# Kernel tuning notes

Measured on AMD Instinct MI355X. Metric: run time of the kernel, lower is better.

Reference implementation:

```python
import jax, jax.numpy as jnp
import numpy as np

B, S, D = 8, 2048, 768        # batch, seq_len, embed_dim
G1, G2, G3 = 16, 16, 16       # grid_shape
L = 768                       # latent_dim
TEMP = 0.5                    # initial temperature (learnable scalar)
GRID_STD = 0.05               # keras 'random_normal' default stddev


def _glorot_uniform(key, fan_in, fan_out):
    lim = jnp.sqrt(6.0 / (fan_in + fan_out))
    return jax.random.uniform(key, (fan_in, fan_out), minval=-lim, maxval=lim, dtype=jnp.float32)


def setup_inputs() -> dict:
    key = jax.random.key(0)
    kx, k1, k2, k3, kg = jax.random.split(key, 5)
    x = jax.random.normal(kx, (B, S, D), dtype=jnp.float32)
    W1 = _glorot_uniform(k1, D, G1)
    W2 = _glorot_uniform(k2, D, G2)
    W3 = _glorot_uniform(k3, D, G3)
    b1 = jnp.zeros((G1,), jnp.float32)
    b2 = jnp.zeros((G2,), jnp.float32)
    b3 = jnp.zeros((G3,), jnp.float32)
    grid = GRID_STD * jax.random.normal(kg, (G1, G2, G3, L), dtype=jnp.float32)
    temperature = jnp.asarray(TEMP, dtype=jnp.float32)
    return {"x": x, "W1": W1, "b1": b1, "W2": W2, "b2": b2,
            "W3": W3, "b3": b3, "grid": grid, "temperature": temperature}


def reference(x, W1, b1, W2, b2, W3, b3, grid, temperature):
    # Flatten (batch, seq) -> tokens, process each token independently (transformer mode)
    b, s, d = x.shape
    xt = x.reshape(b * s, d)                                # (T, D)
    # Per-dimension temperature-controlled softmax addressing distributions
    p1 = jax.nn.softmax((xt @ W1 + b1) / temperature, axis=-1)   # (T, G1)
    p2 = jax.nn.softmax((xt @ W2 + b2) / temperature, axis=-1)   # (T, G2)
    p3 = jax.nn.softmax((xt @ W3 + b3) / temperature, axis=-1)   # (T, G3)
    # Joint probability (outer product) contracted with grid latent vectors:
    # out[t, l] = sum_{i,j,k} p1[t,i] p2[t,j] p3[t,k] grid[i,j,k,l]
    out = jnp.einsum('ti,tj,tk,ijkl->tl', p1, p2, p3, grid, optimize=True)
    return out.reshape(b, s, -1)                            # (B, S, L)
```

## Files before the change

kernel.cpp:

```cpp
#include <hip/hip_runtime.h>
#include <hip/hip_bf16.h>


using f32x2  = __attribute__((ext_vector_type(2))) float;
using f32x4  = __attribute__((ext_vector_type(4))) float;
using f32x16 = __attribute__((ext_vector_type(16))) float;
using half8  = __attribute__((ext_vector_type(8))) _Float16;
using half2v = __attribute__((ext_vector_type(2))) _Float16;
typedef unsigned short ushort_t;
typedef unsigned int uint_t;

typedef const __attribute__((address_space(1))) void* gptr_t;
typedef __attribute__((address_space(3))) void* lptr_t;

#define PSTRIDE 52

static __device__ __forceinline__ ushort_t f2h_bits(float x) {
  union { _Float16 h; ushort_t u; } c;
  c.h = (_Float16)x;
  return c.u;
}

static __device__ __forceinline__ half2v cvt_pkrtz2(float a, float b) {
  auto r = __builtin_amdgcn_cvt_pkrtz(a, b);
  union { decltype(r) i; half2v o; } u;
  u.i = r;
  return u.o;
}

__global__ __launch_bounds__(256) void k_pack(const float* __restrict__ g,
                                              ushort_t* __restrict__ gT,
                                              const float* __restrict__ W1,
                                              const float* __restrict__ W2,
                                              const float* __restrict__ W3,
                                              ushort_t* __restrict__ wfrag) {
  const int tx = threadIdx.x;
  if (blockIdx.y == 12) {
    if (blockIdx.x >= 9) return;
#pragma unroll
    for (int j = 0; j < 16; ++j) {
      const int u = blockIdx.x * 4096 + tx * 16 + j;
      const int e = u & 7;
      const int l = (u >> 3) & 63;
      const int frag = u >> 9;
      const int ks = frag / 3, nf = frag % 3;
      const int d = ks * 32 + 8 * (l >> 4) + e;
      const int col = l & 15;
      const float* Wsel = (nf == 0) ? W1 : (nf == 1) ? W2 : W3;
      wfrag[u] = f2h_bits(Wsel[d * 16 + col]);
    }
    return;
  }
  __shared__ ushort_t tile[64][65];
  const int r0 = blockIdx.x * 64;
  const int c0 = blockIdx.y * 64;
#pragma unroll
  for (int it = 0; it < 4; ++it) {
    const int idx = tx + it * 256;
    const int r = idx >> 4;
    const int c = (idx & 15) << 2;
    const float4 v = *(const float4*)(g + (size_t)(r0 + r) * 768 + (c0 + c));
    tile[c + 0][r] = f2h_bits(v.x);
    tile[c + 1][r] = f2h_bits(v.y);
    tile[c + 2][r] = f2h_bits(v.z);
    tile[c + 3][r] = f2h_bits(v.w);
  }
  __syncthreads();
#pragma unroll
  for (int it = 0; it < 4; ++it) {
    const int idx = tx + it * 256;
    const int r = idx >> 4;
    const int c = (idx & 15) << 2;
    ushort4 o;
    o.x = tile[r][c + 0]; o.y = tile[r][c + 1];
    o.z = tile[r][c + 2]; o.w = tile[r][c + 3];
    *(ushort4*)(gT + (size_t)(c0 + r) * 4096 + (r0 + c)) = o;
  }
}

__global__ __launch_bounds__(256) void k_prep(const float* __restrict__ x,
                                              const ushort_t* __restrict__ wfrag,
                                              const float* __restrict__ b1,
                                              const float* __restrict__ b2,
                                              const float* __restrict__ b3,
                                              const float* __restrict__ temp,
                                              float* __restrict__ p) {
  const int tid = threadIdx.x;
  const int lane = tid & 63;
  const int wv = tid >> 6;
  const int t0w = blockIdx.x * 64 + wv * 16;
  const int m = lane & 15;
  const int q = lane >> 4;

  const float* xrow = x + (size_t)(t0w + m) * 768 + q * 8;

  f32x4 acc[3];
#pragma unroll
  for (int nf = 0; nf < 3; ++nf) acc[nf] = (f32x4){0.f, 0.f, 0.f, 0.f};

  const ushort_t* wf = wfrag + lane * 8;
#pragma unroll
  for (int ks = 0; ks < 24; ++ks) {
    const f32x4 xa = *(const f32x4*)(xrow + ks * 32);
    const f32x4 xb = *(const f32x4*)(xrow + ks * 32 + 4);
    union { half2v h2[4]; half8 h8; } pk;
    pk.h2[0] = cvt_pkrtz2(xa[0], xa[1]);
    pk.h2[1] = cvt_pkrtz2(xa[2], xa[3]);
    pk.h2[2] = cvt_pkrtz2(xb[0], xb[1]);
    pk.h2[3] = cvt_pkrtz2(xb[2], xb[3]);
    const half8 a = pk.h8;
#pragma unroll
    for (int nf = 0; nf < 3; ++nf) {
      const half8 w = *(const half8*)&wf[(size_t)(ks * 3 + nf) * 512];
      acc[nf] = __builtin_amdgcn_mfma_f32_16x16x32_f16(a, w, acc[nf], 0, 0, 0);
    }
  }

  const float invT = 1.0f / temp[0];
  float z[3][4];
  const float bias[3] = {b1[m], b2[m], b3[m]};
#pragma unroll
  for (int nf = 0; nf < 3; ++nf)
#pragma unroll
    for (int r = 0; r < 4; ++r) z[nf][r] = (acc[nf][r] + bias[nf]) * invT;

#pragma unroll
  for (int grp = 0; grp < 3; ++grp) {
    float mx[4], sm[4];
#pragma unroll
    for (int r = 0; r < 4; ++r) mx[r] = z[grp][r];
#pragma unroll
    for (int msk = 1; msk < 16; msk <<= 1)
#pragma unroll
      for (int r = 0; r < 4; ++r) mx[r] = fmaxf(mx[r], __shfl_xor(mx[r], msk));
#pragma unroll
    for (int r = 0; r < 4; ++r) { z[grp][r] = __expf(z[grp][r] - mx[r]); sm[r] = z[grp][r]; }
#pragma unroll
    for (int msk = 1; msk < 16; msk <<= 1)
#pragma unroll
      for (int r = 0; r < 4; ++r) sm[r] += __shfl_xor(sm[r], msk);
#pragma unroll
    for (int r = 0; r < 4; ++r) z[grp][r] /= sm[r];
  }

#pragma unroll
  for (int r = 0; r < 4; ++r) {
    float* prow = p + (size_t)(t0w + 4 * q + r) * PSTRIDE + m;
#pragma unroll
    for (int grp = 0; grp < 3; ++grp) prow[grp * 16] = z[grp][r];
  }
}

__global__ __launch_bounds__(256, 2) void k_gemm(const float* __restrict__ p_g,
                                                 const ushort_t* __restrict__ gT,
                                                 float* __restrict__ out) {
  __shared__ ushort_t Bt[2][192 * 64];
  __shared__ float p1T[16 * 128];

  const int tid = threadIdx.x;
  const int lane = tid & 63;
  const int wv = __builtin_amdgcn_readfirstlane(tid >> 6);
  const int wm = wv >> 1, wn = wv & 1;
  const int g = lane >> 5;
  const int l31 = lane & 31;

  const int f = blockIdx.y * 128 + blockIdx.x;
  const int w = (f & 7) * 64 + (f >> 3);
  const int m0 = (w & 127) * 128;
  const int n0 = (w >> 7) * 192;

  if (tid < 128) {
    const float* pr = p_g + (size_t)(m0 + tid) * PSTRIDE;
#pragma unroll
    for (int qq = 0; qq < 4; ++qq) {
      const f32x4 v = *(const f32x4*)(pr + qq * 4);
#pragma unroll
      for (int e = 0; e < 4; ++e) p1T[(qq * 4 + e) * 128 + tid] = v[e];
    }
  }

  const int rowA0 = m0 + wm * 64 + l31;
  half2v p2h[2][16];
  float p3r[2][8];
#pragma unroll
  for (int mr = 0; mr < 2; ++mr) {
    const float* pr = p_g + (size_t)(rowA0 + mr * 32) * PSTRIDE;
#pragma unroll
    for (int qq = 0; qq < 4; ++qq) {
      const f32x4 v = *(const f32x4*)(pr + 16 + qq * 4);
#pragma unroll
      for (int e = 0; e < 4; ++e)
        p2h[mr][qq * 4 + e] = cvt_pkrtz2(v[e], v[e]);
    }
#pragma unroll
    for (int qq = 0; qq < 2; ++qq) {
      const f32x4 v = *(const f32x4*)(pr + 32 + 8 * g + qq * 4);
      p3r[mr][qq * 4 + 0] = v[0]; p3r[mr][qq * 4 + 1] = v[1];
      p3r[mr][qq * 4 + 2] = v[2]; p3r[mr][qq * 4 + 3] = v[3];
    }
  }

  const int srow = wv * 48 + (lane >> 3);
  const int schunk = (lane & 7) ^ (lane >> 3);
  const ushort_t* sbase = gT + (size_t)(n0 + srow) * 4096 + schunk * 8;
  auto stage = [&](int buf, int kt) {
    const ushort_t* src = sbase + kt * 64;
#pragma unroll
    for (int qq = 0; qq < 6; ++qq) {
      __builtin_amdgcn_global_load_lds((gptr_t)(src + (size_t)qq * 8 * 4096),
                                       (lptr_t)&Bt[buf][(wv * 48 + qq * 8) * 64], 16, 0, 0);
    }
  };

  f32x16 acc[2][3];
#pragma unroll
  for (int mr = 0; mr < 2; ++mr)
#pragma unroll
    for (int nf = 0; nf < 3; ++nf)
#pragma unroll
      for (int e = 0; e < 16; ++e) acc[mr][nf][e] = 0.f;

  stage(0, 0);
  asm volatile("s_waitcnt vmcnt(0) lgkmcnt(0)" ::: "memory");
  __builtin_amdgcn_s_barrier();

  const int rowLoc0 = wm * 64 + l31;
  for (int io = 0; io < 16; ++io) {
    half2v p1p3h[2][4];
#pragma unroll
    for (int mr = 0; mr < 2; ++mr) {
      const float p1v = p1T[io * 128 + rowLoc0 + mr * 32];
#pragma unroll
      for (int qq = 0; qq < 4; ++qq)
        p1p3h[mr][qq] = cvt_pkrtz2(p1v * p3r[mr][2 * qq],
                                   p1v * p3r[mr][2 * qq + 1]);
    }
#pragma unroll
    for (int kq = 0; kq < 4; ++kq) {
      const int kt = io * 4 + kq;
      const ushort_t* bbuf = Bt[kq & 1];

      half8 b[4][3];
#pragma unroll
      for (int s = 0; s < 4; ++s) {
        const int cd = 2 * s + g;
#pragma unroll
        for (int nf = 0; nf < 3; ++nf) {
          const int r = wn * 96 + nf * 32 + l31;
          b[s][nf] = *(const half8*)&bbuf[r * 64 + ((cd ^ (r & 7)) << 3)];
        }
      }
      if (kq < 3 || io < 15) stage((kq + 1) & 1, kt + 1);

#pragma unroll
      for (int s = 0; s < 4; ++s) {
        const int j = kq * 4 + s;
        half8 a[2];
#pragma unroll
        for (int mr = 0; mr < 2; ++mr) {
          union { half2v h2[4]; half8 h8; } pk;
#pragma unroll
          for (int qq = 0; qq < 4; ++qq) pk.h2[qq] = p2h[mr][j] * p1p3h[mr][qq];
          a[mr] = pk.h8;
        }
        __builtin_amdgcn_s_setprio(1);
#pragma unroll
        for (int mr = 0; mr < 2; ++mr)
#pragma unroll
          for (int nf = 0; nf < 3; ++nf)
            acc[mr][nf] = __builtin_amdgcn_mfma_f32_32x32x16_f16(a[mr], b[s][nf], acc[mr][nf], 0, 0, 0);
        __builtin_amdgcn_s_setprio(0);
      }
      asm volatile("s_waitcnt vmcnt(0)" ::: "memory");
      __builtin_amdgcn_s_barrier();
    }
  }

#pragma unroll
  for (int mr = 0; mr < 2; ++mr)
#pragma unroll
    for (int nf = 0; nf < 3; ++nf)
#pragma unroll
      for (int reg = 0; reg < 16; ++reg) {
        const int row = (reg & 3) + 8 * (reg >> 2) + 4 * g;
        const int t = m0 + wm * 64 + mr * 32 + row;
        out[(size_t)t * 768 + n0 + wn * 96 + nf * 32 + l31] = acc[mr][nf][reg];
      }
}

extern "C" void kernel_launch(void* const* d_in, const int* in_sizes, int n_in,
                              void* d_out, int out_size, void* d_ws, size_t ws_size,
                              hipStream_t stream) {
  (void)in_sizes; (void)n_in; (void)out_size; (void)ws_size;
  const float* x    = (const float*)d_in[0];
  const float* W1   = (const float*)d_in[1];
  const float* b1   = (const float*)d_in[2];
  const float* W2   = (const float*)d_in[3];
  const float* b2   = (const float*)d_in[4];
  const float* W3   = (const float*)d_in[5];
  const float* b3   = (const float*)d_in[6];
  const float* grid = (const float*)d_in[7];
  const float* temp = (const float*)d_in[8];
  float* out = (float*)d_out;

  ushort_t* gT = (ushort_t*)d_ws;
  float* p = (float*)((char*)d_ws + 6291456);
  ushort_t* wfrag = (ushort_t*)((char*)d_ws + 6291456 + 3407872);

  k_pack<<<dim3(64, 13), 256, 0, stream>>>(grid, gT, W1, W2, W3, wfrag);
  k_prep<<<dim3(256), 256, 0, stream>>>(x, wfrag, b1, b2, b3, temp, p);
  k_gemm<<<dim3(128, 4), 256, 0, stream>>>(p, gT, out);
}
```

Before: 106.6 us.

## Switch GEMM to single-wave blocks with barrier-free double-buffered staging

The GEMM kernel goes from 256-thread blocks with 128x192 tiles to one wavefront per block with 64x96 tiles and 2048 blocks. With a single wave, the LDS staging of grid fragments needs no s_barrier and relies only on vmcnt waits, with a smaller 32-wide K step and a matching swizzle. p1 is also stored as fp16 in LDS. This removes cross-wave synchronisation and gives more blocks to fill the CUs. The cost is less reuse of the B tile per load, so grid traffic from L2 rises, and there are more per-block prologue loads.

```diff
diff --git a/kernel.cpp b/kernel.cpp
--- a/kernel.cpp
+++ b/kernel.cpp
@@ -151,40 +151,35 @@
   }
 }
 
-__global__ __launch_bounds__(256, 2) void k_gemm(const float* __restrict__ p_g,
-                                                 const ushort_t* __restrict__ gT,
-                                                 float* __restrict__ out) {
-  __shared__ ushort_t Bt[2][192 * 64];
-  __shared__ float p1T[16 * 128];
-
-  const int tid = threadIdx.x;
-  const int lane = tid & 63;
-  const int wv = __builtin_amdgcn_readfirstlane(tid >> 6);
-  const int wm = wv >> 1, wn = wv & 1;
+__global__ __launch_bounds__(64) void k_gemm(const float* __restrict__ p_g,
+                                             const ushort_t* __restrict__ gT,
+                                             float* __restrict__ out) {
+  __shared__ ushort_t Bt[2][96 * 32];
+  __shared__ ushort_t p1h[16 * 64];
+
+  const int lane = threadIdx.x;
   const int g = lane >> 5;
   const int l31 = lane & 31;
 
-  const int f = blockIdx.y * 128 + blockIdx.x;
-  const int w = (f & 7) * 64 + (f >> 3);
-  const int m0 = (w & 127) * 128;
-  const int n0 = (w >> 7) * 192;
-
-  if (tid < 128) {
-    const float* pr = p_g + (size_t)(m0 + tid) * PSTRIDE;
+  const int f = blockIdx.x;
+  const int m0 = (f >> 3) * 64;
+  const int n0 = (f & 7) * 96;
+
+  {
+    const float* pr = p_g + (size_t)(m0 + lane) * PSTRIDE;
 #pragma unroll
     for (int qq = 0; qq < 4; ++qq) {
       const f32x4 v = *(const f32x4*)(pr + qq * 4);
 #pragma unroll
-      for (int e = 0; e < 4; ++e) p1T[(qq * 4 + e) * 128 + tid] = v[e];
-    }
-  }
-
-  const int rowA0 = m0 + wm * 64 + l31;
+      for (int e = 0; e < 4; ++e) p1h[(qq * 4 + e) * 64 + lane] = f2h_bits(v[e]);
+    }
+  }
+
   half2v p2h[2][16];
   float p3r[2][8];
 #pragma unroll
   for (int mr = 0; mr < 2; ++mr) {
-    const float* pr = p_g + (size_t)(rowA0 + mr * 32) * PSTRIDE;
+    const float* pr = p_g + (size_t)(m0 + mr * 32 + l31) * PSTRIDE;
 #pragma unroll
     for (int qq = 0; qq < 4; ++qq) {
       const f32x4 v = *(const f32x4*)(pr + 16 + qq * 4);
@@ -200,15 +195,15 @@
     }
   }
 
-  const int srow = wv * 48 + (lane >> 3);
-  const int schunk = (lane & 7) ^ (lane >> 3);
+  const int srow = lane >> 2;
+  const int schunk = (lane & 3) ^ ((lane >> 3) & 3);
   const ushort_t* sbase = gT + (size_t)(n0 + srow) * 4096 + schunk * 8;
   auto stage = [&](int buf, int kt) {
-    const ushort_t* src = sbase + kt * 64;
-#pragma unroll
-    for (int qq = 0; qq < 6; ++qq) {
-      __builtin_amdgcn_global_load_lds((gptr_t)(src + (size_t)qq * 8 * 4096),
-                                       (lptr_t)&Bt[buf][(wv * 48 + qq * 8) * 64], 16, 0, 0);
+    const ushort_t* src = sbase + kt * 32;
+#pragma unroll
+    for (int q = 0; q < 6; ++q) {
+      __builtin_amdgcn_global_load_lds((gptr_t)(src + (size_t)q * 16 * 4096),
+                                       (lptr_t)&Bt[buf][q * 512], 16, 0, 0);
     }
   };
 
@@ -221,40 +216,42 @@
       for (int e = 0; e < 16; ++e) acc[mr][nf][e] = 0.f;
 
   stage(0, 0);
-  asm volatile("s_waitcnt vmcnt(0) lgkmcnt(0)" ::: "memory");
-  __builtin_amdgcn_s_barrier();
-
-  const int rowLoc0 = wm * 64 + l31;
+
+  const int rsw = (l31 >> 1) & 3;
+
   for (int io = 0; io < 16; ++io) {
     half2v p1p3h[2][4];
 #pragma unroll
     for (int mr = 0; mr < 2; ++mr) {
-      const float p1v = p1T[io * 128 + rowLoc0 + mr * 32];
+      union { ushort_t u; _Float16 h; } c;
+      c.u = p1h[io * 64 + mr * 32 + l31];
+      const float p1v = (float)c.h;
 #pragma unroll
       for (int qq = 0; qq < 4; ++qq)
         p1p3h[mr][qq] = cvt_pkrtz2(p1v * p3r[mr][2 * qq],
                                    p1v * p3r[mr][2 * qq + 1]);
     }
 #pragma unroll
-    for (int kq = 0; kq < 4; ++kq) {
-      const int kt = io * 4 + kq;
-      const ushort_t* bbuf = Bt[kq & 1];
-
-      half8 b[4][3];
-#pragma unroll
-      for (int s = 0; s < 4; ++s) {
+    for (int u = 0; u < 8; ++u) {
+      const int kt = io * 8 + u;
+      if (kt < 127) {
+        stage((u & 1) ^ 1, kt + 1);
+        asm volatile("s_waitcnt vmcnt(6)" ::: "memory");
+      } else {
+        asm volatile("s_waitcnt vmcnt(0)" ::: "memory");
+      }
+      const ushort_t* bbuf = Bt[u & 1];
+
+#pragma unroll
+      for (int s = 0; s < 2; ++s) {
         const int cd = 2 * s + g;
+        half8 b[3];
 #pragma unroll
         for (int nf = 0; nf < 3; ++nf) {
-          const int r = wn * 96 + nf * 32 + l31;
-          b[s][nf] = *(const half8*)&bbuf[r * 64 + ((cd ^ (r & 7)) << 3)];
+          const int r = nf * 32 + l31;
+          b[nf] = *(const half8*)&bbuf[r * 32 + ((cd ^ rsw) << 3)];
         }
-      }
-      if (kq < 3 || io < 15) stage((kq + 1) & 1, kt + 1);
-
-#pragma unroll
-      for (int s = 0; s < 4; ++s) {
-        const int j = kq * 4 + s;
+        const int j = (2 * u + s) & 15;
         half8 a[2];
 #pragma unroll
         for (int mr = 0; mr < 2; ++mr) {
@@ -268,11 +265,9 @@
         for (int mr = 0; mr < 2; ++mr)
 #pragma unroll
           for (int nf = 0; nf < 3; ++nf)
-            acc[mr][nf] = __builtin_amdgcn_mfma_f32_32x32x16_f16(a[mr], b[s][nf], acc[mr][nf], 0, 0, 0);
+            acc[mr][nf] = __builtin_amdgcn_mfma_f32_32x32x16_f16(a[mr], b[nf], acc[mr][nf], 0, 0, 0);
         __builtin_amdgcn_s_setprio(0);
       }
-      asm volatile("s_waitcnt vmcnt(0)" ::: "memory");
-      __builtin_amdgcn_s_barrier();
     }
   }
 
@@ -283,8 +278,8 @@
 #pragma unroll
       for (int reg = 0; reg < 16; ++reg) {
         const int row = (reg & 3) + 8 * (reg >> 2) + 4 * g;
-        const int t = m0 + wm * 64 + mr * 32 + row;
-        out[(size_t)t * 768 + n0 + wn * 96 + nf * 32 + l31] = acc[mr][nf][reg];
+        const int t = m0 + mr * 32 + row;
+        out[(size_t)t * 768 + n0 + nf * 32 + l31] = acc[mr][nf][reg];
       }
 }
 
@@ -309,5 +304,5 @@
 
   k_pack<<<dim3(64, 13), 256, 0, stream>>>(grid, gT, W1, W2, W3, wfrag);
   k_prep<<<dim3(256), 256, 0, stream>>>(x, wfrag, b1, b2, b3, temp, p);
-  k_gemm<<<dim3(128, 4), 256, 0, stream>>>(p, gT, out);
-}
+  k_gemm<<<dim3(2048), 64, 0, stream>>>(p, gT, out);
+}
```

Result: slower. 128.7 us (+20.8%).
